# Performance work log

Measured on AMD Instinct MI355X. Metric: run time of the kernel, lower is better.

## Reference

```python
import jax, jax.numpy as jnp
import numpy as np

D_MODEL = 1024
N_HEADS = 16
HEAD_DIM = D_MODEL // N_HEADS
THETA = 10000.0
NEG = -1e9


def apply_rope(x, positions, theta=THETA):
    # x: (B, H, S, d), positions: (B, 1, S)
    d = x.shape[-1]
    inv_freq = 1.0 / (theta ** (jnp.arange(0, d, 2, dtype=jnp.float32) / d))  # (d/2,)
    freqs = positions[..., None].astype(jnp.float32) * inv_freq  # (B, 1, S, d/2)
    cos, sin = jnp.cos(freqs), jnp.sin(freqs)
    xr = x.reshape(x.shape[:-1] + (d // 2, 2))
    xe, xo = xr[..., 0], xr[..., 1]
    rot = jnp.stack([xe * cos - xo * sin, xe * sin + xo * cos], axis=-1)
    return rot.reshape(x.shape)


def setup_inputs() -> dict:
    key = jax.random.key(0)
    ks = jax.random.split(key, 5)
    B, S = 2, 2048
    scale = 1.0 / np.sqrt(D_MODEL)
    return {
        "x": jax.random.normal(ks[0], (B, S, D_MODEL), dtype=jnp.float32),
        "wq": jax.random.normal(ks[1], (D_MODEL, D_MODEL), dtype=jnp.float32) * scale,
        "wk": jax.random.normal(ks[2], (D_MODEL, D_MODEL), dtype=jnp.float32) * scale,
        "wv": jax.random.normal(ks[3], (D_MODEL, D_MODEL), dtype=jnp.float32) * scale,
        "wo": jax.random.normal(ks[4], (D_MODEL, D_MODEL), dtype=jnp.float32) * scale,
        "token_positions": jnp.arange(S, dtype=jnp.int64),
    }


def reference(x, wq, wk, wv, wo, token_positions):
    B, S, D = x.shape
    H, d = N_HEADS, HEAD_DIM
    # QKV projections (module does x @ w.T)
    q = (x @ wq.T).reshape(B, S, H, d).transpose(0, 2, 1, 3)  # (B, H, S, d)
    k = (x @ wk.T).reshape(B, S, H, d).transpose(0, 2, 1, 3)
    v = (x @ wv.T).reshape(B, S, H, d).transpose(0, 2, 1, 3)
    pos = jnp.broadcast_to(token_positions[None, :], (B, S))[:, None, :]  # (B, 1, S)
    q = apply_rope(q, pos)
    k = apply_rope(k, pos)
    scores = jnp.einsum("bhqd,bhkd->bhqk", q, k) / jnp.sqrt(jnp.float32(d))
    causal = jnp.tril(jnp.ones((S, S), dtype=bool))
    scores = jnp.where(causal[None, None], scores, NEG)
    attn = jax.nn.softmax(scores, axis=-1)
    out = jnp.einsum("bhqk,bhkd->bhqd", attn, v)
    out = out.transpose(0, 2, 1, 3).reshape(B, S, D)
    return out @ wo.T
```

## Files before the change

kernel.cpp:

```cpp
#include <hip/hip_runtime.h>

typedef __bf16 bf16;
typedef __bf16 bf16x8 __attribute__((ext_vector_type(8)));
typedef __bf16 bf16x4 __attribute__((ext_vector_type(4)));
typedef float f32x4 __attribute__((ext_vector_type(4)));
typedef float f32x16 __attribute__((ext_vector_type(16)));
typedef float fx2 __attribute__((ext_vector_type(2)));

#define DEV static __device__ __forceinline__

constexpr int BB = 2, SS = 2048, DM = 1024, NH = 16, HD = 64;
constexpr int MTOT = BB * SS;
constexpr float LOG2E = 1.4426950408889634f;

constexpr size_t OFF_XB   = 0;
constexpr size_t OFF_WQKV = OFF_XB   + (size_t)MTOT * DM * 2;
constexpr size_t OFF_WO   = OFF_WQKV + (size_t)3 * DM * DM * 2;
constexpr size_t OFF_TAB  = OFF_WO   + (size_t)DM * DM * 2;
constexpr size_t OFF_Q    = OFF_TAB  + (size_t)SS * (HD/2) * 8;
constexpr size_t OFF_K    = OFF_Q    + (size_t)MTOT * DM * 2;
constexpr size_t OFF_VT   = OFF_K    + (size_t)MTOT * DM * 2;
constexpr size_t OFF_AO   = OFF_VT   + (size_t)MTOT * DM * 2;

typedef const __attribute__((address_space(1))) void gas_void;
typedef __attribute__((address_space(3))) void las_void;

DEV void gload16(const bf16* g, bf16* l) {
  __builtin_amdgcn_global_load_lds((gas_void*)g, (las_void*)l, 16, 0, 0);
}

DEV f32x4 mfma16(bf16x8 a, bf16x8 b, f32x4 c) {
  return __builtin_amdgcn_mfma_f32_16x16x32_bf16(a, b, c, 0, 0, 0);
}

DEV f32x16 mfma32(bf16x8 a, bf16x8 b, f32x16 c) {
  return __builtin_amdgcn_mfma_f32_32x32x16_bf16(a, b, c, 0, 0, 0);
}

DEV unsigned pack2(float a, float b) {
  union { bf16 h[2]; unsigned u; } cv;
  cv.h[0] = (bf16)a; cv.h[1] = (bf16)b;
  return cv.u;
}

__global__ void prep_kernel(const float* __restrict__ x, const float* __restrict__ wq,
    const float* __restrict__ wk, const float* __restrict__ wv, const float* __restrict__ wo,
    const int* __restrict__ pos, bf16* __restrict__ xb, bf16* __restrict__ wqkv,
    bf16* __restrict__ wob, fx2* __restrict__ tab) {
  const int NX4 = MTOT * DM / 4;
  const int NW4 = DM * DM / 4;
  const int TOTC = NX4 + 4 * NW4;
  const int NTAB = SS * (HD / 2);
  const int total = TOTC + NTAB;
  for (int i = blockIdx.x * blockDim.x + threadIdx.x; i < total; i += gridDim.x * blockDim.x) {
    if (i < TOTC) {
      const float* src; bf16* dst; int off;
      if (i < NX4) { src = x; dst = xb; off = i; }
      else {
        int i2 = i - NX4; int which = i2 >> 18; off = i2 & (NW4 - 1);
        src = which == 0 ? wq : which == 1 ? wk : which == 2 ? wv : wo;
        dst = which == 0 ? wqkv : which == 1 ? wqkv + DM * DM : which == 2 ? wqkv + 2 * DM * DM : wob;
      }
      float4 v = ((const float4*)src)[off];
      bf16x4 o4 = { (bf16)v.x, (bf16)v.y, (bf16)v.z, (bf16)v.w };
      ((bf16x4*)dst)[off] = o4;
    } else {
      int e = i - TOTC;
      int s = e >> 5, p = e & 31;
      float invf = __builtin_exp2f(-(float)p * (13.287712379549449f / 32.0f));
      float ang = (float)pos[s] * invf;
      fx2 cs; cs.x = cosf(ang); cs.y = sinf(ang);
      tab[e] = cs;
    }
  }
}

DEV void gemm_bt_128(const bf16* __restrict__ A, const bf16* __restrict__ Bw,
                     int rowA0, int rowB0, f32x4 (&acc)[4][4]) {
  __shared__ __align__(16) bf16 lA[128 * 32];
  __shared__ __align__(16) bf16 lB[128 * 32];
  const int t = threadIdx.x, w = t >> 6, lane = t & 63;
  const int wr = w >> 1, wc = w & 1, g = lane >> 4, c = lane & 15;
#pragma unroll
  for (int mi = 0; mi < 4; mi++)
#pragma unroll
    for (int ni = 0; ni < 4; ni++) acc[mi][ni] = (f32x4){0.f, 0.f, 0.f, 0.f};
  const bf16* ga = A + (size_t)(rowA0 + (t >> 2)) * DM + (t & 3) * 8;
  const bf16* gb = Bw + (size_t)(rowB0 + (t >> 2)) * DM + (t & 3) * 8;
  bf16* la = lA + w * 512;
  bf16* lb = lB + w * 512;
  const int arow = wr * 64 + c, brow = wc * 64 + c;
  for (int k0 = 0; k0 < DM; k0 += 32) {
    gload16(ga + k0,            la);
    gload16(ga + k0 + 64 * DM,  la + 2048);
    gload16(gb + k0,            lb);
    gload16(gb + k0 + 64 * DM,  lb + 2048);
    __syncthreads();
    bf16x8 af[4], bf_[4];
#pragma unroll
    for (int mi = 0; mi < 4; mi++) af[mi]  = *(const bf16x8*)(lA + (arow + mi * 16) * 32 + g * 8);
#pragma unroll
    for (int ni = 0; ni < 4; ni++) bf_[ni] = *(const bf16x8*)(lB + (brow + ni * 16) * 32 + g * 8);
#pragma unroll
    for (int mi = 0; mi < 4; mi++)
#pragma unroll
      for (int ni = 0; ni < 4; ni++)
        acc[mi][ni] = mfma16(af[mi], bf_[ni], acc[mi][ni]);
    __syncthreads();
  }
}

__global__ __launch_bounds__(256, 2) void qkv_kernel(const bf16* __restrict__ xb,
    const bf16* __restrict__ wqkv, const fx2* __restrict__ tab,
    bf16* __restrict__ Qb, bf16* __restrict__ Kb, bf16* __restrict__ VTb) {
  f32x4 acc[4][4];
  const int rowA0 = blockIdx.y * 128, rowB0 = blockIdx.x * 128;
  gemm_bt_128(xb, wqkv, rowA0, rowB0, acc);
  const int t = threadIdx.x, w = t >> 6, lane = t & 63;
  const int wr = w >> 1, wc = w & 1, g = lane >> 4, c = lane & 15;
  const int which = rowB0 >> 10;
#pragma unroll
  for (int mi = 0; mi < 4; mi++)
#pragma unroll
    for (int ni = 0; ni < 4; ni++) {
      const int ncol = rowB0 + wc * 64 + ni * 16 + c;
      const int nn = ncol & (DM - 1), h = nn >> 6, dd = nn & 63;
#pragma unroll
      for (int j = 0; j < 4; j++) {
        const int mrow = rowA0 + wr * 64 + mi * 16 + 4 * g + j;
        const int b = mrow >> 11, s = mrow & (SS - 1);
        float v = acc[mi][ni][j];
        if (which < 2) {
          float partner = __shfl_xor(v, 1);
          fx2 cs = tab[s * 32 + (dd >> 1)];
          v = v * cs.x + ((dd & 1) ? partner : -partner) * cs.y;
          bf16* dst = which == 0 ? Qb : Kb;
          dst[((size_t)((b * NH + h) * SS + s)) * HD + dd] = (bf16)v;
        } else {
          VTb[((size_t)((b * NH + h) * HD + dd)) * SS + s] = (bf16)v;
        }
      }
    }
}

__global__ __launch_bounds__(64, 2) void attn_kernel(const bf16* __restrict__ Q,
    const bf16* __restrict__ K, const bf16* __restrict__ VT, bf16* __restrict__ AO) {
  __shared__ __align__(16) unsigned char smem[16384];
  const int flat = blockIdx.x;
  const int flat2 = (flat & 7) * 128 + (flat >> 3);
  const int bh = flat2 >> 5;
  const int p = flat2 & 31;
  const int lane = threadIdx.x & 63;
  const int q31 = lane & 31, hi = lane >> 5;
  const bf16* Qp = Q + (size_t)bh * SS * HD;
  const bf16* Kp = K + (size_t)bh * SS * HD;
  const bf16* Vp = VT + (size_t)bh * HD * SS;
  const float SCL = 0.125f * LOG2E;

  const bf16* kSrcBase = Kp + (size_t)(lane >> 3) * HD + ((lane & 7) ^ (lane >> 3)) * 8;
  auto stageK = [&](int k0, unsigned koff) {
    const bf16* src = kSrcBase + (size_t)k0 * HD;
    bf16* dst = (bf16*)(smem + koff);
#pragma unroll
    for (int i = 0; i < 8; i++)
      gload16(src + i * 8 * HD, dst + i * 512);
  };

  auto run_chunk = [&](int qbase, int nt) {
    bf16x8 qb[4];
#pragma unroll
    for (int ds = 0; ds < 4; ds++) {
      bf16x8 xq = *(const bf16x8*)(Qp + (size_t)(qbase + q31) * HD + ds * 16 + hi * 8);
#pragma unroll
      for (int e = 0; e < 8; e++) xq[e] = (bf16)((float)xq[e] * SCL);
      qb[ds] = xq;
    }
    float m_r = -3.0e38f, lsum = 0.f;
    f32x16 o0, o1;
#pragma unroll
    for (int e = 0; e < 16; e++) { o0[e] = 0.f; o1[e] = 0.f; }

    stageK(0, 0);
    unsigned cur = 0;
    for (int tv = 0; tv < nt; ++tv) {
      const int k0 = tv * 64;
      asm volatile("s_waitcnt vmcnt(0)" ::: "memory");
      __builtin_amdgcn_sched_barrier(0);
      f32x16 s0, s1;
#pragma unroll
      for (int e = 0; e < 16; e++) { s0[e] = 0.f; s1[e] = 0.f; }
      {
        const unsigned rowb0 = cur * 8192 + q31 * 128;
        const unsigned sw = (unsigned)(q31 & 7) << 4;
#pragma unroll
        for (int ds = 0; ds < 4; ds++) {
          const unsigned co = (((unsigned)(ds * 2 + hi)) << 4) ^ sw;
          bf16x8 kf0 = *(const bf16x8*)(smem + rowb0 + co);
          bf16x8 kf1 = *(const bf16x8*)(smem + rowb0 + 4096 + co);
          s0 = mfma32(kf0, qb[ds], s0);
          s1 = mfma32(kf1, qb[ds], s1);
        }
      }
      bf16x8 vf[2][4];
#pragma unroll
      for (int dt = 0; dt < 2; dt++)
#pragma unroll
        for (int ks = 0; ks < 4; ks++)
          vf[dt][ks] = *(const bf16x8*)(Vp + (size_t)(dt * 32 + q31) * SS + k0 + ks * 16 + hi * 8);
      if (tv + 1 < nt) stageK(k0 + 64, (cur ^ 1) * 8192);
      if (k0 + 63 > qbase) {
        const int qg = qbase + q31;
#pragma unroll
        for (int r = 0; r < 16; r++) {
          const int kg = k0 + (r & 3) + 8 * (r >> 2) + 4 * hi;
          if (kg > qg)      s0[r] = -1.0e30f;
          if (kg + 32 > qg) s1[r] = -1.0e30f;
        }
      }
      float pm = s0[0];
#pragma unroll
      for (int r = 1; r < 16; r++) pm = fmaxf(pm, s0[r]);
#pragma unroll
      for (int r = 0; r < 16; r++) pm = fmaxf(pm, s1[r]);
      pm = fmaxf(pm, __shfl_xor(pm, 32));
      const float mnew = fmaxf(m_r, pm);
      const float alpha = __builtin_exp2f(m_r - mnew);
      float rs = 0.f;
#pragma unroll
      for (int r = 0; r < 16; r++) {
        s0[r] = __builtin_exp2f(s0[r] - mnew); rs += s0[r];
        s1[r] = __builtin_exp2f(s1[r] - mnew); rs += s1[r];
      }
      rs += __shfl_xor(rs, 32);
      lsum = alpha * lsum + rs;
      m_r = mnew;
#pragma unroll
      for (int e = 0; e < 16; e++) { o0[e] *= alpha; o1[e] *= alpha; }
      bf16x8 pf[4];
#pragma unroll
      for (int ks = 0; ks < 4; ks++) {
        const int rb = 8 * (ks & 1);
        float va0, va1, va2, va3, vb0, vb1, vb2, vb3;
        if (ks < 2) {
          va0 = s0[rb]; va1 = s0[rb + 1]; va2 = s0[rb + 2]; va3 = s0[rb + 3];
          vb0 = s0[rb + 4]; vb1 = s0[rb + 5]; vb2 = s0[rb + 6]; vb3 = s0[rb + 7];
        } else {
          va0 = s1[rb]; va1 = s1[rb + 1]; va2 = s1[rb + 2]; va3 = s1[rb + 3];
          vb0 = s1[rb + 4]; vb1 = s1[rb + 5]; vb2 = s1[rb + 6]; vb3 = s1[rb + 7];
        }
        const unsigned a01 = pack2(va0, va1), a23 = pack2(va2, va3);
        const unsigned b01 = pack2(vb0, vb1), b23 = pack2(vb2, vb3);
        const unsigned z1 = (unsigned)__shfl_xor((int)(hi ? a01 : b01), 32);
        const unsigned z2 = (unsigned)__shfl_xor((int)(hi ? a23 : b23), 32);
        union { unsigned u[4]; bf16x8 v; } cv;
        cv.u[0] = hi ? z1 : a01;
        cv.u[1] = hi ? z2 : a23;
        cv.u[2] = hi ? b01 : z1;
        cv.u[3] = hi ? b23 : z2;
        pf[ks] = cv.v;
      }
#pragma unroll
      for (int ks = 0; ks < 4; ks++) {
        o0 = mfma32(vf[0][ks], pf[ks], o0);
        o1 = mfma32(vf[1][ks], pf[ks], o1);
      }
      cur ^= 1;
    }
    const float inv = 1.0f / lsum;
    const int b = bh >> 4, h = bh & 15;
    const size_t rowb = ((size_t)(b * SS + qbase + q31)) * DM + h * HD;
#pragma unroll
    for (int g2 = 0; g2 < 4; g2++) {
      bf16x4 w0, w1;
#pragma unroll
      for (int j = 0; j < 4; j++) {
        w0[j] = (bf16)(o0[4 * g2 + j] * inv);
        w1[j] = (bf16)(o1[4 * g2 + j] * inv);
      }
      *(bf16x4*)(AO + rowb +      8 * g2 + 4 * hi) = w0;
      *(bf16x4*)(AO + rowb + 32 + 8 * g2 + 4 * hi) = w1;
    }
  };

  run_chunk(p * 32, p / 2 + 1);
  const int ph = 63 - p;
  run_chunk(ph * 32, ph / 2 + 1);
}

__global__ __launch_bounds__(256, 2) void oproj_kernel(const bf16* __restrict__ AO,
    const bf16* __restrict__ wob, float* __restrict__ out) {
  f32x4 acc[4][4];
  const int rowA0 = blockIdx.y * 128, rowB0 = blockIdx.x * 128;
  gemm_bt_128(AO, wob, rowA0, rowB0, acc);
  const int t = threadIdx.x, w = t >> 6, lane = t & 63;
  const int wr = w >> 1, wc = w & 1, g = lane >> 4, c = lane & 15;
#pragma unroll
  for (int mi = 0; mi < 4; mi++)
#pragma unroll
    for (int ni = 0; ni < 4; ni++) {
      const int ncol = rowB0 + wc * 64 + ni * 16 + c;
#pragma unroll
      for (int j = 0; j < 4; j++) {
        const int mrow = rowA0 + wr * 64 + mi * 16 + 4 * g + j;
        out[(size_t)mrow * DM + ncol] = acc[mi][ni][j];
      }
    }
}

extern "C" void kernel_launch(void* const* d_in, const int* in_sizes, int n_in,
                              void* d_out, int out_size, void* d_ws, size_t ws_size,
                              hipStream_t stream) {
  const float* x  = (const float*)d_in[0];
  const float* wq = (const float*)d_in[1];
  const float* wk = (const float*)d_in[2];
  const float* wv = (const float*)d_in[3];
  const float* wo = (const float*)d_in[4];
  const int*   pos = (const int*)d_in[5];
  char* ws = (char*)d_ws;
  bf16* xb   = (bf16*)(ws + OFF_XB);
  bf16* wqkv = (bf16*)(ws + OFF_WQKV);
  bf16* wob  = (bf16*)(ws + OFF_WO);
  fx2*  tab  = (fx2*)(ws + OFF_TAB);
  bf16* Qb   = (bf16*)(ws + OFF_Q);
  bf16* Kb   = (bf16*)(ws + OFF_K);
  bf16* VTb  = (bf16*)(ws + OFF_VT);
  bf16* AOb  = (bf16*)(ws + OFF_AO);

  hipLaunchKernelGGL(prep_kernel, dim3(2048), dim3(256), 0, stream,
                     x, wq, wk, wv, wo, pos, xb, wqkv, wob, tab);
  hipLaunchKernelGGL(qkv_kernel, dim3(24, 32), dim3(256), 0, stream,
                     xb, wqkv, tab, Qb, Kb, VTb);
  hipLaunchKernelGGL(attn_kernel, dim3(1024), dim3(64), 0, stream,
                     Qb, Kb, VTb, AOb);
  hipLaunchKernelGGL(oproj_kernel, dim3(8, 32), dim3(256), 0, stream,
                     AOb, wob, (float*)d_out);
}
```

Measured before the change: 138.2 us.

## Split attention into one chunk per block, heaviest-first, with lazy softmax rescale

The attention kernel now launches one block per 32-row query chunk instead of pairing a light and a heavy chunk in one block. Blocks are ordered so the longest causal chunks are scheduled first, which gives more parallelism and better load balancing. The online softmax now skips the rescale of the running max and accumulators unless some lane's max grows by more than 8 in log2 units. The row max and row sum are also computed with tree reductions to shorten dependency chains. The lazy rescale lets exp values exceed 1 (up to 2^8), which slightly raises the risk of bf16 precision loss.

Measured after the change: 160.2 us. 1.16x slower.

```diff
diff --git a/kernel.cpp b/kernel.cpp
--- a/kernel.cpp
+++ b/kernel.cpp
@@ -147,15 +147,17 @@
     const bf16* __restrict__ K, const bf16* __restrict__ VT, bf16* __restrict__ AO) {
   __shared__ __align__(16) unsigned char smem[16384];
   const int flat = blockIdx.x;
-  const int flat2 = (flat & 7) * 128 + (flat >> 3);
-  const int bh = flat2 >> 5;
-  const int p = flat2 & 31;
+  const int flat2 = (flat & 7) * 256 + (flat >> 3);
+  const int bh = flat2 >> 6;
+  const int ci = 63 - (flat2 & 63);
   const int lane = threadIdx.x & 63;
   const int q31 = lane & 31, hi = lane >> 5;
   const bf16* Qp = Q + (size_t)bh * SS * HD;
   const bf16* Kp = K + (size_t)bh * SS * HD;
   const bf16* Vp = VT + (size_t)bh * HD * SS;
   const float SCL = 0.125f * LOG2E;
+  const int qbase = ci * 32;
+  const int nt = ci / 2 + 1;
 
   const bf16* kSrcBase = Kp + (size_t)(lane >> 3) * HD + ((lane & 7) ^ (lane >> 3)) * 8;
   auto stageK = [&](int k0, unsigned koff) {
@@ -166,125 +168,130 @@
       gload16(src + i * 8 * HD, dst + i * 512);
   };
 
-  auto run_chunk = [&](int qbase, int nt) {
-    bf16x8 qb[4];
-#pragma unroll
-    for (int ds = 0; ds < 4; ds++) {
-      bf16x8 xq = *(const bf16x8*)(Qp + (size_t)(qbase + q31) * HD + ds * 16 + hi * 8);
-#pragma unroll
-      for (int e = 0; e < 8; e++) xq[e] = (bf16)((float)xq[e] * SCL);
-      qb[ds] = xq;
-    }
-    float m_r = -3.0e38f, lsum = 0.f;
-    f32x16 o0, o1;
-#pragma unroll
-    for (int e = 0; e < 16; e++) { o0[e] = 0.f; o1[e] = 0.f; }
-
-    stageK(0, 0);
-    unsigned cur = 0;
-    for (int tv = 0; tv < nt; ++tv) {
-      const int k0 = tv * 64;
-      asm volatile("s_waitcnt vmcnt(0)" ::: "memory");
-      __builtin_amdgcn_sched_barrier(0);
-      f32x16 s0, s1;
-#pragma unroll
-      for (int e = 0; e < 16; e++) { s0[e] = 0.f; s1[e] = 0.f; }
-      {
-        const unsigned rowb0 = cur * 8192 + q31 * 128;
-        const unsigned sw = (unsigned)(q31 & 7) << 4;
-#pragma unroll
-        for (int ds = 0; ds < 4; ds++) {
-          const unsigned co = (((unsigned)(ds * 2 + hi)) << 4) ^ sw;
-          bf16x8 kf0 = *(const bf16x8*)(smem + rowb0 + co);
-          bf16x8 kf1 = *(const bf16x8*)(smem + rowb0 + 4096 + co);
-          s0 = mfma32(kf0, qb[ds], s0);
-          s1 = mfma32(kf1, qb[ds], s1);
-        }
-      }
-      bf16x8 vf[2][4];
-#pragma unroll
-      for (int dt = 0; dt < 2; dt++)
-#pragma unroll
-        for (int ks = 0; ks < 4; ks++)
-          vf[dt][ks] = *(const bf16x8*)(Vp + (size_t)(dt * 32 + q31) * SS + k0 + ks * 16 + hi * 8);
-      if (tv + 1 < nt) stageK(k0 + 64, (cur ^ 1) * 8192);
-      if (k0 + 63 > qbase) {
-        const int qg = qbase + q31;
-#pragma unroll
-        for (int r = 0; r < 16; r++) {
-          const int kg = k0 + (r & 3) + 8 * (r >> 2) + 4 * hi;
-          if (kg > qg)      s0[r] = -1.0e30f;
-          if (kg + 32 > qg) s1[r] = -1.0e30f;
-        }
-      }
-      float pm = s0[0];
-#pragma unroll
-      for (int r = 1; r < 16; r++) pm = fmaxf(pm, s0[r]);
-#pragma unroll
-      for (int r = 0; r < 16; r++) pm = fmaxf(pm, s1[r]);
-      pm = fmaxf(pm, __shfl_xor(pm, 32));
-      const float mnew = fmaxf(m_r, pm);
-      const float alpha = __builtin_exp2f(m_r - mnew);
-      float rs = 0.f;
+  bf16x8 qb[4];
+#pragma unroll
+  for (int ds = 0; ds < 4; ds++) {
+    bf16x8 xq = *(const bf16x8*)(Qp + (size_t)(qbase + q31) * HD + ds * 16 + hi * 8);
+#pragma unroll
+    for (int e = 0; e < 8; e++) xq[e] = (bf16)((float)xq[e] * SCL);
+    qb[ds] = xq;
+  }
+  float m_r = -3.0e38f, lsum = 0.f;
+  f32x16 o0, o1;
+#pragma unroll
+  for (int e = 0; e < 16; e++) { o0[e] = 0.f; o1[e] = 0.f; }
+
+  stageK(0, 0);
+  unsigned cur = 0;
+  for (int tv = 0; tv < nt; ++tv) {
+    const int k0 = tv * 64;
+    asm volatile("s_waitcnt vmcnt(0)" ::: "memory");
+    __builtin_amdgcn_sched_barrier(0);
+    f32x16 s0, s1;
+#pragma unroll
+    for (int e = 0; e < 16; e++) { s0[e] = 0.f; s1[e] = 0.f; }
+    {
+      const unsigned rowb0 = cur * 8192 + q31 * 128;
+      const unsigned sw = (unsigned)(q31 & 7) << 4;
+#pragma unroll
+      for (int ds = 0; ds < 4; ds++) {
+        const unsigned co = (((unsigned)(ds * 2 + hi)) << 4) ^ sw;
+        bf16x8 kf0 = *(const bf16x8*)(smem + rowb0 + co);
+        bf16x8 kf1 = *(const bf16x8*)(smem + rowb0 + 4096 + co);
+        s0 = mfma32(kf0, qb[ds], s0);
+        s1 = mfma32(kf1, qb[ds], s1);
+      }
+    }
+    bf16x8 vf[2][4];
+#pragma unroll
+    for (int dt = 0; dt < 2; dt++)
+#pragma unroll
+      for (int ks = 0; ks < 4; ks++)
+        vf[dt][ks] = *(const bf16x8*)(Vp + (size_t)(dt * 32 + q31) * SS + k0 + ks * 16 + hi * 8);
+    if (tv + 1 < nt) stageK(k0 + 64, (cur ^ 1) * 8192);
+    if (k0 + 63 > qbase) {
+      const int qg = qbase + q31;
 #pragma unroll
       for (int r = 0; r < 16; r++) {
-        s0[r] = __builtin_exp2f(s0[r] - mnew); rs += s0[r];
-        s1[r] = __builtin_exp2f(s1[r] - mnew); rs += s1[r];
-      }
-      rs += __shfl_xor(rs, 32);
-      lsum = alpha * lsum + rs;
-      m_r = mnew;
-#pragma unroll
-      for (int e = 0; e < 16; e++) { o0[e] *= alpha; o1[e] *= alpha; }
-      bf16x8 pf[4];
-#pragma unroll
-      for (int ks = 0; ks < 4; ks++) {
-        const int rb = 8 * (ks & 1);
-        float va0, va1, va2, va3, vb0, vb1, vb2, vb3;
-        if (ks < 2) {
-          va0 = s0[rb]; va1 = s0[rb + 1]; va2 = s0[rb + 2]; va3 = s0[rb + 3];
-          vb0 = s0[rb + 4]; vb1 = s0[rb + 5]; vb2 = s0[rb + 6]; vb3 = s0[rb + 7];
-        } else {
-          va0 = s1[rb]; va1 = s1[rb + 1]; va2 = s1[rb + 2]; va3 = s1[rb + 3];
-          vb0 = s1[rb + 4]; vb1 = s1[rb + 5]; vb2 = s1[rb + 6]; vb3 = s1[rb + 7];
-        }
-        const unsigned a01 = pack2(va0, va1), a23 = pack2(va2, va3);
-        const unsigned b01 = pack2(vb0, vb1), b23 = pack2(vb2, vb3);
-        const unsigned z1 = (unsigned)__shfl_xor((int)(hi ? a01 : b01), 32);
-        const unsigned z2 = (unsigned)__shfl_xor((int)(hi ? a23 : b23), 32);
-        union { unsigned u[4]; bf16x8 v; } cv;
-        cv.u[0] = hi ? z1 : a01;
-        cv.u[1] = hi ? z2 : a23;
-        cv.u[2] = hi ? b01 : z1;
-        cv.u[3] = hi ? b23 : z2;
-        pf[ks] = cv.v;
-      }
-#pragma unroll
-      for (int ks = 0; ks < 4; ks++) {
-        o0 = mfma32(vf[0][ks], pf[ks], o0);
-        o1 = mfma32(vf[1][ks], pf[ks], o1);
-      }
-      cur ^= 1;
-    }
-    const float inv = 1.0f / lsum;
-    const int b = bh >> 4, h = bh & 15;
-    const size_t rowb = ((size_t)(b * SS + qbase + q31)) * DM + h * HD;
-#pragma unroll
-    for (int g2 = 0; g2 < 4; g2++) {
-      bf16x4 w0, w1;
-#pragma unroll
-      for (int j = 0; j < 4; j++) {
-        w0[j] = (bf16)(o0[4 * g2 + j] * inv);
-        w1[j] = (bf16)(o1[4 * g2 + j] * inv);
-      }
-      *(bf16x4*)(AO + rowb +      8 * g2 + 4 * hi) = w0;
-      *(bf16x4*)(AO + rowb + 32 + 8 * g2 + 4 * hi) = w1;
-    }
-  };
-
-  run_chunk(p * 32, p / 2 + 1);
-  const int ph = 63 - p;
-  run_chunk(ph * 32, ph / 2 + 1);
+        const int kg = k0 + (r & 3) + 8 * (r >> 2) + 4 * hi;
+        if (kg > qg)      s0[r] = -1.0e30f;
+        if (kg + 32 > qg) s1[r] = -1.0e30f;
+      }
+    }
+    {
+      float a[16];
+#pragma unroll
+      for (int r = 0; r < 16; r++) a[r] = fmaxf(s0[r], s1[r]);
+#pragma unroll
+      for (int d = 8; d > 0; d >>= 1)
+#pragma unroll
+        for (int r = 0; r < d; r++) a[r] = fmaxf(a[r], a[r + d]);
+      const float pm = fmaxf(a[0], __shfl_xor(a[0], 32));
+      if (__any(pm > m_r + 8.0f)) {
+        const float mnew = fmaxf(m_r, pm);
+        const float alpha = __builtin_exp2f(m_r - mnew);
+        lsum *= alpha;
+#pragma unroll
+        for (int e = 0; e < 16; e++) { o0[e] *= alpha; o1[e] *= alpha; }
+        m_r = mnew;
+      }
+      float b[16];
+#pragma unroll
+      for (int r = 0; r < 16; r++) {
+        s0[r] = __builtin_exp2f(s0[r] - m_r);
+        s1[r] = __builtin_exp2f(s1[r] - m_r);
+        b[r] = s0[r] + s1[r];
+      }
+#pragma unroll
+      for (int d = 8; d > 0; d >>= 1)
+#pragma unroll
+        for (int r = 0; r < d; r++) b[r] += b[r + d];
+      lsum += b[0] + __shfl_xor(b[0], 32);
+    }
+    bf16x8 pf[4];
+#pragma unroll
+    for (int ks = 0; ks < 4; ks++) {
+      const int rb = 8 * (ks & 1);
+      float va0, va1, va2, va3, vb0, vb1, vb2, vb3;
+      if (ks < 2) {
+        va0 = s0[rb]; va1 = s0[rb + 1]; va2 = s0[rb + 2]; va3 = s0[rb + 3];
+        vb0 = s0[rb + 4]; vb1 = s0[rb + 5]; vb2 = s0[rb + 6]; vb3 = s0[rb + 7];
+      } else {
+        va0 = s1[rb]; va1 = s1[rb + 1]; va2 = s1[rb + 2]; va3 = s1[rb + 3];
+        vb0 = s1[rb + 4]; vb1 = s1[rb + 5]; vb2 = s1[rb + 6]; vb3 = s1[rb + 7];
+      }
+      const unsigned a01 = pack2(va0, va1), a23 = pack2(va2, va3);
+      const unsigned b01 = pack2(vb0, vb1), b23 = pack2(vb2, vb3);
+      const unsigned z1 = (unsigned)__shfl_xor((int)(hi ? a01 : b01), 32);
+      const unsigned z2 = (unsigned)__shfl_xor((int)(hi ? a23 : b23), 32);
+      union { unsigned u[4]; bf16x8 v; } cv;
+      cv.u[0] = hi ? z1 : a01;
+      cv.u[1] = hi ? z2 : a23;
+      cv.u[2] = hi ? b01 : z1;
+      cv.u[3] = hi ? b23 : z2;
+      pf[ks] = cv.v;
+    }
+#pragma unroll
+    for (int ks = 0; ks < 4; ks++) {
+      o0 = mfma32(vf[0][ks], pf[ks], o0);
+      o1 = mfma32(vf[1][ks], pf[ks], o1);
+    }
+    cur ^= 1;
+  }
+  const float inv = 1.0f / lsum;
+  const int b = bh >> 4, h = bh & 15;
+  const size_t rowb = ((size_t)(b * SS + qbase + q31)) * DM + h * HD;
+#pragma unroll
+  for (int g2 = 0; g2 < 4; g2++) {
+    bf16x4 w0, w1;
+#pragma unroll
+    for (int j = 0; j < 4; j++) {
+      w0[j] = (bf16)(o0[4 * g2 + j] * inv);
+      w1[j] = (bf16)(o1[4 * g2 + j] * inv);
+    }
+    *(bf16x4*)(AO + rowb +      8 * g2 + 4 * hi) = w0;
+    *(bf16x4*)(AO + rowb + 32 + 8 * g2 + 4 * hi) = w1;
+  }
 }
 
 __global__ __launch_bounds__(256, 2) void oproj_kernel(const bf16* __restrict__ AO,
@@ -330,7 +337,7 @@
                      x, wq, wk, wv, wo, pos, xb, wqkv, wob, tab);
   hipLaunchKernelGGL(qkv_kernel, dim3(24, 32), dim3(256), 0, stream,
                      xb, wqkv, tab, Qb, Kb, VTb);
-  hipLaunchKernelGGL(attn_kernel, dim3(1024), dim3(64), 0, stream,
+  hipLaunchKernelGGL(attn_kernel, dim3(2048), dim3(64), 0, stream,
                      Qb, Kb, VTb, AOb);
   hipLaunchKernelGGL(oproj_kernel, dim3(8, 32), dim3(256), 0, stream,
                      AOb, wob, (float*)d_out);
```
